# Performance work log

Measured on AMD Instinct MI355X. Metric: run time of the kernel, lower is better.

Reference implementation:

```python
import jax, jax.numpy as jnp
import numpy as np

B, N = 8192, 128          # batch, num intruders
D_OWN, D_GRID, D_INTR = 16, 512, 20
H, OUT = 128, 4


def setup_inputs() -> dict:
    key = jax.random.key(0)
    ks = jax.random.split(key, 12)
    rn = lambda k, shape, s=1.0: jax.random.normal(k, shape, jnp.float32) * s
    return {
        "state0": rn(ks[0], (B, D_OWN)),
        "state1": rn(ks[1], (B, D_GRID)),
        "state2": rn(ks[2], (B, N, D_INTR)),
        "W_own": rn(ks[3], (D_OWN, H), 0.1), "b_own": jnp.zeros((H,), jnp.float32),
        "W_intr": rn(ks[4], (D_INTR, H), 0.1), "b_intr": jnp.zeros((H,), jnp.float32),
        "W_grid": rn(ks[5], (D_GRID, H), 0.05), "b_grid": jnp.zeros((H,), jnp.float32),
        "Wq": rn(ks[6], (H, H), 0.08),
        "Wk": rn(ks[7], (H, H), 0.08),
        "Wv": rn(ks[8], (H, H), 0.08),
        "W1": rn(ks[9], (3 * H, H), 0.05), "b1": jnp.zeros((H,), jnp.float32),
        "W2": rn(ks[10], (H, OUT), 0.1), "b2": jnp.zeros((OUT,), jnp.float32),
    }


def reference(state0, state1, state2, W_own, b_own, W_intr, b_intr,
              W_grid, b_grid, Wq, Wk, Wv, W1, b1, W2, b2):
    own_e = jax.nn.relu(state0 @ W_own + b_own)            # [B,H]
    x_e = jax.nn.relu(state2 @ W_intr + b_intr)            # [B,N,H]
    q = own_e @ Wq                                         # [B,H]
    k = x_e @ Wk                                           # [B,N,H]
    v = x_e @ Wv                                           # [B,N,H]
    # mask = state2.mean(axis=2, keepdim=True).bool()  (nonzero test)
    mask = jnp.mean(state2, axis=2, keepdims=True) != 0    # [B,N,1]
    score = jnp.einsum('bnh,bh->bn', k, q)[..., None]      # bmm(k, q.unsqueeze(2)) -> [B,N,1]
    score = jnp.where(mask, score, -jnp.inf)
    alpha = jax.nn.softmax(score / np.float32(np.sqrt(H)), axis=1)
    alpha = jnp.where(mask, alpha, 0.0)
    v_att = jnp.sum(v * alpha, axis=1)                     # [B,H]
    own_grid = jax.nn.relu(state1 @ W_grid + b_grid)       # [B,H]
    concat = jnp.concatenate([own_e, v_att, own_grid], axis=1)  # [B,3H]
    out = (concat @ W1 + b1) @ W2 + b2                     # action_out_SAC
    mean = out
    log_std = jnp.clip(out, -20.0, 2.0)
    return mean, log_std
```

## Files before the change

kernel.cpp:

```cpp
#include <hip/hip_runtime.h>

typedef unsigned short ushort_t;
typedef __attribute__((ext_vector_type(8))) short bf16x8;
typedef __attribute__((ext_vector_type(4))) float f32x4;

__device__ __forceinline__ float bflo(unsigned u) { return __uint_as_float(u << 16); }
__device__ __forceinline__ float bfhi(unsigned u) { return __uint_as_float(u & 0xffff0000u); }
__device__ __forceinline__ float bfu(ushort_t s)  { return __uint_as_float((unsigned)s << 16); }
__device__ __forceinline__ ushort_t f2bf(float f) {
    unsigned u = __float_as_uint(f);
    u = u + 0x7fffu + ((u >> 16) & 1u);
    return (ushort_t)(u >> 16);
}
__device__ __forceinline__ void unpack8(uint4 v, float* f) {
    f[0]=bflo(v.x); f[1]=bfhi(v.x); f[2]=bflo(v.y); f[3]=bfhi(v.y);
    f[4]=bflo(v.z); f[5]=bfhi(v.z); f[6]=bflo(v.w); f[7]=bfhi(v.w);
}

__device__ __forceinline__ float load1(const void* p, size_t i, int f32) {
    return f32 ? ((const float*)p)[i] : bfu(((const ushort_t*)p)[i]);
}
__device__ __forceinline__ void load8(const void* p, size_t i, int f32, float* f) {
    if (f32) {
        const float4 a = *(const float4*)((const float*)p + i);
        const float4 b = *(const float4*)((const float*)p + i + 4);
        f[0]=a.x; f[1]=a.y; f[2]=a.z; f[3]=a.w;
        f[4]=b.x; f[5]=b.y; f[6]=b.z; f[7]=b.w;
    } else {
        unpack8(*(const uint4*)((const ushort_t*)p + i), f);
    }
}
__device__ __forceinline__ void load4(const void* p, size_t i, int f32, float* f) {
    if (f32) {
        const float4 a = *(const float4*)((const float*)p + i);
        f[0]=a.x; f[1]=a.y; f[2]=a.z; f[3]=a.w;
    } else {
        const uint2 u = *(const uint2*)((const ushort_t*)p + i);
        f[0]=bflo(u.x); f[1]=bfhi(u.x); f[2]=bflo(u.y); f[3]=bfhi(u.y);
    }
}

__device__ __forceinline__ int detect_f32(const ushort_t* s1h) {
    const int ln = threadIdx.x & 63;
    float v = fmaxf(fabsf(bfu(s1h[ln])), fabsf(bfu(s1h[ln + 64])));
    bool big = !(v <= 1e6f);
    return __ballot(big) != 0ull;
}

#define B_TOT 8192

__device__ __attribute__((aligned(16))) float    g_M[128 * 128];
__device__ __attribute__((aligned(16))) float    g_Wc1[384 * 4];
__device__ __attribute__((aligned(16))) float    g_Wv2[128 * 4];
__device__ __attribute__((aligned(16))) float    g_bc[4];
__device__ __attribute__((aligned(16))) float    g_t[B_TOT * 128];
__device__ __attribute__((aligned(16))) float    g_ogc[B_TOT * 4];
__device__ __attribute__((aligned(16))) ushort_t g_oe[B_TOT * 128];
__device__ __attribute__((aligned(16))) ushort_t g_Wib[128 * 32];

__global__ __launch_bounds__(128) void k_pre(
    const void* __restrict__ Wq, const void* __restrict__ Wk,
    const void* __restrict__ Wv, const void* __restrict__ W1,
    const void* __restrict__ b1, const void* __restrict__ W2,
    const void* __restrict__ b2, const void* __restrict__ W_intr,
    const ushort_t* __restrict__ s1h)
{
    __shared__ float wq_sh[128];
    __shared__ float w2_sh[512];
    __shared__ float wc1_mid[512];
    __shared__ float redc[128][4];
    const int tid = threadIdx.x;
    const int bx = blockIdx.x;
    const int f32 = detect_f32(s1h);

    if (bx < 128) {
        wq_sh[tid] = load1(Wq, bx*128 + tid, f32);
        __syncthreads();
        float acc = 0.f;
        #pragma unroll
        for (int c = 0; c < 16; ++c) {
            float f[8]; load8(Wk, (size_t)tid*128 + c*8, f32, f);
            #pragma unroll
            for (int j = 0; j < 8; ++j) acc = fmaf(wq_sh[c*8+j], f[j], acc);
        }
        g_M[bx*128 + tid] = acc;
    } else if (bx < 131) {
        const int rbase = (bx - 128) * 128;
        for (int i = tid; i < 512; i += 128) w2_sh[i] = load1(W2, i, f32);
        __syncthreads();

        const int r = rbase + tid;
        float a[4] = {0.f, 0.f, 0.f, 0.f};
        #pragma unroll
        for (int c = 0; c < 16; ++c) {
            float f[8]; load8(W1, (size_t)r*128 + c*8, f32, f);
            #pragma unroll
            for (int j = 0; j < 8; ++j) {
                const int p = c*8 + j;
                #pragma unroll
                for (int q = 0; q < 4; ++q) a[q] = fmaf(f[j], w2_sh[p*4+q], a[q]);
            }
        }
        #pragma unroll
        for (int q = 0; q < 4; ++q) g_Wc1[r*4+q] = a[q];

        if (bx == 129) {
            #pragma unroll
            for (int q = 0; q < 4; ++q) wc1_mid[tid*4+q] = a[q];
            __syncthreads();
            float v[4] = {0.f, 0.f, 0.f, 0.f};
            #pragma unroll
            for (int c = 0; c < 16; ++c) {
                float f[8]; load8(Wv, (size_t)tid*128 + c*8, f32, f);
                #pragma unroll
                for (int j = 0; j < 8; ++j) {
                    const int i2 = c*8 + j;
                    #pragma unroll
                    for (int q = 0; q < 4; ++q) v[q] = fmaf(f[j], wc1_mid[i2*4+q], v[q]);
                }
            }
            #pragma unroll
            for (int q = 0; q < 4; ++q) g_Wv2[tid*4+q] = v[q];

            const float bv = load1(b1, tid, f32);
            #pragma unroll
            for (int q = 0; q < 4; ++q) redc[tid][q] = bv * w2_sh[tid*4+q];
            __syncthreads();
            for (int s = 64; s > 0; s >>= 1) {
                if (tid < s) {
                    #pragma unroll
                    for (int q = 0; q < 4; ++q) redc[tid][q] += redc[tid+s][q];
                }
                __syncthreads();
            }
            if (tid < 4) g_bc[tid] = redc[0][tid] + load1(b2, tid, f32);
        }
    } else {
        ushort_t row[32];
        #pragma unroll
        for (int k = 0; k < 20; ++k) row[k] = f2bf(load1(W_intr, (size_t)k*128 + tid, f32));
        #pragma unroll
        for (int k = 20; k < 32; ++k) row[k] = 0;
        uint4* dst = (uint4*)&g_Wib[tid*32];
        const uint4* src = (const uint4*)row;
        #pragma unroll
        for (int c = 0; c < 4; ++c) dst[c] = src[c];
    }
}

__global__ __launch_bounds__(256) void k_ownt(
    const void* __restrict__ state0, const void* __restrict__ W_own,
    const void* __restrict__ b_own, const ushort_t* __restrict__ s1h)
{
    __shared__ float s0sh[16*16];
    __shared__ float wosh[16*128];
    __shared__ float bosh[128];
    __shared__ float oesh[16*129];
    __shared__ float Mt[32][128];
    const int tid = threadIdx.x;
    const int b0 = blockIdx.x * 16;
    const int f32 = detect_f32(s1h);

    if (tid < 32) {
        float f[8]; load8(state0, (size_t)b0*16 + tid*8, f32, f);
        #pragma unroll
        for (int j = 0; j < 8; ++j) s0sh[tid*8 + j] = f[j];
    }
    {
        float f[8]; load8(W_own, (size_t)tid*8, f32, f);
        #pragma unroll
        for (int j = 0; j < 8; ++j) wosh[tid*8 + j] = f[j];
    }
    if (tid < 128) bosh[tid] = load1(b_own, tid, f32);
    __syncthreads();

    #pragma unroll
    for (int kk = 0; kk < 8; ++kk) {
        const int idx = tid + kk*256;
        const int bi = idx >> 7, h = idx & 127;
        float acc = bosh[h];
        #pragma unroll
        for (int d = 0; d < 16; ++d) acc = fmaf(s0sh[bi*16+d], wosh[d*128+h], acc);
        acc = fmaxf(acc, 0.f);
        oesh[bi*129 + h] = acc;
        g_oe[(size_t)(b0+bi)*128 + h] = f2bf(acc);
    }

    const int bi0 = (tid >> 5) * 2;
    const int h0  = (tid & 31) * 4;
    float t00=0.f,t01=0.f,t02=0.f,t03=0.f,t10=0.f,t11=0.f,t12=0.f,t13=0.f;
    for (int kt = 0; kt < 128; kt += 32) {
        __syncthreads();
        #pragma unroll
        for (int c = 0; c < 4; ++c) {
            const int i = tid + c*256;
            const int kk = i >> 5;
            const int hh = (i & 31) * 4;
            *(float4*)&Mt[kk][hh] = *(const float4*)&g_M[(size_t)(kt+kk)*128 + hh];
        }
        __syncthreads();
        #pragma unroll
        for (int k = 0; k < 32; ++k) {
            const float4 mv = *(const float4*)&Mt[k][h0];
            const float a0 = oesh[(bi0+0)*129 + kt + k];
            const float a1 = oesh[(bi0+1)*129 + kt + k];
            t00=fmaf(a0,mv.x,t00); t01=fmaf(a0,mv.y,t01); t02=fmaf(a0,mv.z,t02); t03=fmaf(a0,mv.w,t03);
            t10=fmaf(a1,mv.x,t10); t11=fmaf(a1,mv.y,t11); t12=fmaf(a1,mv.z,t12); t13=fmaf(a1,mv.w,t13);
        }
    }
    *(float4*)&g_t[(size_t)(b0+bi0+0)*128 + h0] = make_float4(t00,t01,t02,t03);
    *(float4*)&g_t[(size_t)(b0+bi0+1)*128 + h0] = make_float4(t10,t11,t12,t13);
}

__global__ __launch_bounds__(256) void k_grid(
    const void* __restrict__ state1, const void* __restrict__ W_grid,
    const void* __restrict__ b_grid)
{
    __shared__ float s1T[32][18];
    __shared__ float wg[32][128];
    __shared__ float part[32][16][4];
    const int tid = threadIdx.x;
    const int b0 = blockIdx.x * 16;
    const int f32 = detect_f32((const ushort_t*)state1);

    const int bq = tid & 7;
    const int hq = tid >> 3;
    float a00=0.f,a01=0.f,a02=0.f,a03=0.f;
    float a10=0.f,a11=0.f,a12=0.f,a13=0.f;

    for (int kt = 0; kt < 512; kt += 32) {
        if (kt) __syncthreads();
        if (tid < 128) {
            const int bb = tid >> 3;
            const int kk = (tid & 7) * 4;
            float f[4];
            load4(state1, (size_t)(b0 + bb)*512 + kt + kk, f32, f);
            #pragma unroll
            for (int j = 0; j < 4; ++j) s1T[kk + j][bb] = f[j];
        }
        {
            #pragma unroll
            for (int c = 0; c < 4; ++c) {
                const int i = tid + c*256;
                const int kk = i >> 5;
                const int hh = (i & 31) * 4;
                float f[4];
                load4(W_grid, (size_t)(kt + kk)*128 + hh, f32, f);
                *(float4*)&wg[kk][hh] = make_float4(f[0], f[1], f[2], f[3]);
            }
        }
        __syncthreads();
        #pragma unroll 8
        for (int k = 0; k < 32; ++k) {
            const float x0 = s1T[k][bq*2 + 0];
            const float x1 = s1T[k][bq*2 + 1];
            const float4 w = *(const float4*)&wg[k][hq*4];
            a00=fmaf(x0,w.x,a00); a01=fmaf(x0,w.y,a01); a02=fmaf(x0,w.z,a02); a03=fmaf(x0,w.w,a03);
            a10=fmaf(x1,w.x,a10); a11=fmaf(x1,w.y,a11); a12=fmaf(x1,w.z,a12); a13=fmaf(x1,w.w,a13);
        }
    }

    float accs[2][4] = {{a00,a01,a02,a03},{a10,a11,a12,a13}};
    float pr[2][4] = {{0,0,0,0},{0,0,0,0}};
    #pragma unroll
    for (int jh = 0; jh < 4; ++jh) {
        const int h = hq*4 + jh;
        const float bg = load1(b_grid, h, f32);
        const float4 wc = *(const float4*)&g_Wc1[(256 + h)*4];
        #pragma unroll
        for (int ib = 0; ib < 2; ++ib) {
            const float og = fmaxf(accs[ib][jh] + bg, 0.f);
            pr[ib][0] = fmaf(og, wc.x, pr[ib][0]);
            pr[ib][1] = fmaf(og, wc.y, pr[ib][1]);
            pr[ib][2] = fmaf(og, wc.z, pr[ib][2]);
            pr[ib][3] = fmaf(og, wc.w, pr[ib][3]);
        }
    }
    __syncthreads();
    #pragma unroll
    for (int j = 0; j < 4; ++j) {
        part[hq][bq*2+0][j] = pr[0][j];
        part[hq][bq*2+1][j] = pr[1][j];
    }
    __syncthreads();
    if (tid < 64) {
        const int bb = tid >> 2, j = tid & 3;
        float s = 0.f;
        #pragma unroll
        for (int q = 0; q < 32; ++q) s += part[q][bb][j];
        g_ogc[(size_t)(b0 + bb)*4 + j] = s;
    }
}

__global__ __launch_bounds__(256, 4) void k_main(
    const void* __restrict__ state2, const void* __restrict__ b_intr,
    const ushort_t* __restrict__ s1h, void* __restrict__ out_raw)
{
    __shared__ __attribute__((aligned(16))) ushort_t s2b[128*40];
    __shared__ __attribute__((aligned(16))) ushort_t wib[128*40];
    __shared__ float t_sh[128], oe_sh[128], bi_sh[128];
    __shared__ float2 mlg_sh[128];
    __shared__ float msk_f[128];
    __shared__ float sc_part[4][128];
    __shared__ float u_sh[128];
    __shared__ float red4[4][4];

    const int tid = threadIdx.x;
    const int b = blockIdx.x;
    const int f32 = detect_f32(s1h);
    const int wv = tid >> 6, ln = tid & 63, lq = ln >> 4, lc = ln & 15;

    if (tid < 128) {
        const int n = tid;
        float v[20];
        const size_t base = (size_t)b*2560 + n*20;
        #pragma unroll
        for (int c = 0; c < 5; ++c) load4(state2, base + c*4, f32, v + c*4);
        float ms = 0.f;
        #pragma unroll
        for (int d = 0; d < 20; ++d) ms += v[d];
        msk_f[n] = (ms != 0.f) ? 1.f : 0.f;
        unsigned* row = (unsigned*)&s2b[n*40];
        #pragma unroll
        for (int c = 0; c < 10; ++c)
            row[c] = (unsigned)f2bf(v[2*c]) | ((unsigned)f2bf(v[2*c+1]) << 16);
        #pragma unroll
        for (int c = 10; c < 16; ++c) row[c] = 0u;
        t_sh[n]  = g_t[(size_t)b*128 + n];
        oe_sh[n] = bfu(g_oe[(size_t)b*128 + n]);
        bi_sh[n] = load1(b_intr, n, f32);
    } else {
        const int h = tid - 128;
        const uint4* src = (const uint4*)&g_Wib[h*32];
        uint4* dst = (uint4*)&wib[h*40];
        #pragma unroll
        for (int c = 0; c < 4; ++c) dst[c] = src[c];
    }
    __syncthreads();

    const int ht0 = 2*wv, ht1 = 2*wv + 1;
    const bf16x8 bb0 = *(const bf16x8*)&wib[(ht0*16 + lc)*40 + lq*8];
    const bf16x8 bb1 = *(const bf16x8*)&wib[(ht1*16 + lc)*40 + lq*8];
    const f32x4 zf = {0.f, 0.f, 0.f, 0.f};
    f32x4 acc0[8], acc1[8];
    #pragma unroll
    for (int nt = 0; nt < 8; ++nt) {
        const bf16x8 af = *(const bf16x8*)&s2b[(nt*16 + lc)*40 + lq*8];
        acc0[nt] = __builtin_amdgcn_mfma_f32_16x16x32_bf16(af, bb0, zf, 0, 0, 0);
        acc1[nt] = __builtin_amdgcn_mfma_f32_16x16x32_bf16(af, bb1, zf, 0, 0, 0);
    }

    const float bh0 = bi_sh[ht0*16 + lc], bh1 = bi_sh[ht1*16 + lc];
    const float tv0 = t_sh[ht0*16 + lc],  tv1 = t_sh[ht1*16 + lc];
    #pragma unroll
    for (int nt = 0; nt < 8; ++nt) {
        float s[4];
        #pragma unroll
        for (int r = 0; r < 4; ++r) {
            const float x0 = fmaxf(acc0[nt][r] + bh0, 0.f);
            const float x1 = fmaxf(acc1[nt][r] + bh1, 0.f);
            acc0[nt][r] = x0; acc1[nt][r] = x1;
            s[r] = fmaf(x1, tv1, x0 * tv0);
        }
        #pragma unroll
        for (int off = 1; off < 16; off <<= 1) {
            #pragma unroll
            for (int r = 0; r < 4; ++r) s[r] += __shfl_xor(s[r], off);
        }
        if (lc == 0) {
            #pragma unroll
            for (int r = 0; r < 4; ++r) sc_part[wv][nt*16 + lq*4 + r] = s[r];
        }
    }
    __syncthreads();

    if (tid < 128) {
        const int n = tid;
        const float s = sc_part[0][n] + sc_part[1][n] + sc_part[2][n] + sc_part[3][n];
        const float mk = msk_f[n];
        mlg_sh[n] = make_float2((mk != 0.f) ? s * 0.08838834764831845f : -1e30f, mk);
    }
    __syncthreads();

    const float l0 = mlg_sh[ln].x, l1 = mlg_sh[ln + 64].x;
    float mx = fmaxf(l0, l1);
    #pragma unroll
    for (int off = 1; off < 64; off <<= 1) mx = fmaxf(mx, __shfl_xor(mx, off));
    float es = __expf(fmaxf(l0 - mx, -80.f)) + __expf(fmaxf(l1 - mx, -80.f));
    #pragma unroll
    for (int off = 1; off < 64; off <<= 1) es += __shfl_xor(es, off);
    const float inv_d = 1.f / es;

    float u0 = 0.f, u1 = 0.f;
    #pragma unroll
    for (int nt = 0; nt < 8; ++nt) {
        #pragma unroll
        for (int r = 0; r < 4; ++r) {
            const float2 mlg = mlg_sh[nt*16 + lq*4 + r];
            const float a = mlg.y * __expf(fmaxf(mlg.x - mx, -80.f)) * inv_d;
            u0 = fmaf(a, acc0[nt][r], u0);
            u1 = fmaf(a, acc1[nt][r], u1);
        }
    }
    u0 += __shfl_xor(u0, 16); u0 += __shfl_xor(u0, 32);
    u1 += __shfl_xor(u1, 16); u1 += __shfl_xor(u1, 32);
    if (ln < 16) {
        u_sh[ht0*16 + ln] = u0;
        u_sh[ht1*16 + ln] = u1;
    }
    __syncthreads();

    float c0=0.f, c1=0.f, c2=0.f, c3=0.f;
    if (tid < 128) {
        const int h = tid;
        const float uu = u_sh[h], oo = oe_sh[h];
        const float4 wv2 = *(const float4*)&g_Wv2[h*4];
        const float4 wca = *(const float4*)&g_Wc1[h*4];
        c0 = uu*wv2.x + oo*wca.x;
        c1 = uu*wv2.y + oo*wca.y;
        c2 = uu*wv2.z + oo*wca.z;
        c3 = uu*wv2.w + oo*wca.w;
    }
    #pragma unroll
    for (int off = 32; off > 0; off >>= 1) {
        c0 += __shfl_down(c0, off); c1 += __shfl_down(c1, off);
        c2 += __shfl_down(c2, off); c3 += __shfl_down(c3, off);
    }
    if ((tid & 63) == 0) {
        red4[wv][0]=c0; red4[wv][1]=c1; red4[wv][2]=c2; red4[wv][3]=c3;
    }
    __syncthreads();
    if (tid < 4) {
        const int j = tid;
        const float o = g_bc[j] + g_ogc[(size_t)b*4 + j]
                      + red4[0][j] + red4[1][j] + red4[2][j] + red4[3][j];
        const float ls = fminf(fmaxf(o, -20.f), 2.f);
        if (f32) {
            float* of = (float*)out_raw;
            of[(size_t)b*4 + j] = o;
            of[(size_t)B_TOT*4 + (size_t)b*4 + j] = ls;
        } else {
            ushort_t* os = (ushort_t*)out_raw;
            os[(size_t)b*4 + j] = f2bf(o);
            os[(size_t)B_TOT*4 + (size_t)b*4 + j] = f2bf(ls);
        }
    }
}

extern "C" void kernel_launch(void* const* d_in, const int* in_sizes, int n_in,
                              void* d_out, int out_size, void* d_ws, size_t ws_size,
                              hipStream_t stream)
{
    (void)in_sizes; (void)n_in; (void)out_size; (void)d_ws; (void)ws_size;
    const void* state0 = d_in[0];
    const void* state1 = d_in[1];
    const void* state2 = d_in[2];
    const void* W_own  = d_in[3];
    const void* b_own  = d_in[4];
    const void* W_intr = d_in[5];
    const void* b_intr = d_in[6];
    const void* W_grid = d_in[7];
    const void* b_grid = d_in[8];
    const void* Wq     = d_in[9];
    const void* Wk     = d_in[10];
    const void* Wv     = d_in[11];
    const void* W1     = d_in[12];
    const void* b1     = d_in[13];
    const void* W2     = d_in[14];
    const void* b2     = d_in[15];
    const ushort_t* s1h = (const ushort_t*)state1;

    k_pre  <<<dim3(132), dim3(128), 0, stream>>>(Wq, Wk, Wv, W1, b1, W2, b2,
                                                 W_intr, s1h);
    k_ownt <<<dim3(512), dim3(256), 0, stream>>>(state0, W_own, b_own, s1h);
    k_grid <<<dim3(512), dim3(256), 0, stream>>>(state1, W_grid, b_grid);
    k_main <<<dim3(8192), dim3(256), 0, stream>>>(state2, b_intr, s1h, d_out);
}
```

Baseline: 313.5 us.

## Fuse all four kernels into one per-16-row kernel with per-block weight prep

New measurement: 395.6 us. 26.2% more time.

```diff
diff --git a/kernel.cpp b/kernel.cpp
--- a/kernel.cpp
+++ b/kernel.cpp
@@ -12,11 +12,13 @@
     u = u + 0x7fffu + ((u >> 16) & 1u);
     return (ushort_t)(u >> 16);
 }
+__device__ __forceinline__ unsigned pk2(float a, float b) {
+    return (unsigned)f2bf(a) | ((unsigned)f2bf(b) << 16);
+}
 __device__ __forceinline__ void unpack8(uint4 v, float* f) {
     f[0]=bflo(v.x); f[1]=bfhi(v.x); f[2]=bflo(v.y); f[3]=bfhi(v.y);
     f[4]=bflo(v.z); f[5]=bfhi(v.z); f[6]=bflo(v.w); f[7]=bfhi(v.w);
 }
-
 __device__ __forceinline__ float load1(const void* p, size_t i, int f32) {
     return f32 ? ((const float*)p)[i] : bfu(((const ushort_t*)p)[i]);
 }
@@ -39,7 +41,6 @@
         f[0]=bflo(u.x); f[1]=bfhi(u.x); f[2]=bflo(u.y); f[3]=bfhi(u.y);
     }
 }
-
 __device__ __forceinline__ int detect_f32(const ushort_t* s1h) {
     const int ln = threadIdx.x & 63;
     float v = fmaxf(fabsf(bfu(s1h[ln])), fabsf(bfu(s1h[ln + 64])));
@@ -49,118 +50,108 @@
 
 #define B_TOT 8192
 
-__device__ __attribute__((aligned(16))) float    g_M[128 * 128];
-__device__ __attribute__((aligned(16))) float    g_Wc1[384 * 4];
-__device__ __attribute__((aligned(16))) float    g_Wv2[128 * 4];
-__device__ __attribute__((aligned(16))) float    g_bc[4];
-__device__ __attribute__((aligned(16))) float    g_t[B_TOT * 128];
-__device__ __attribute__((aligned(16))) float    g_ogc[B_TOT * 4];
-__device__ __attribute__((aligned(16))) ushort_t g_oe[B_TOT * 128];
-__device__ __attribute__((aligned(16))) ushort_t g_Wib[128 * 32];
-
-__global__ __launch_bounds__(128) void k_pre(
-    const void* __restrict__ Wq, const void* __restrict__ Wk,
-    const void* __restrict__ Wv, const void* __restrict__ W1,
-    const void* __restrict__ b1, const void* __restrict__ W2,
-    const void* __restrict__ b2, const void* __restrict__ W_intr,
-    const ushort_t* __restrict__ s1h)
+__global__ __launch_bounds__(256, 2) void k_fused(
+    const void* __restrict__ state0, const void* __restrict__ state1,
+    const void* __restrict__ state2, const void* __restrict__ W_own,
+    const void* __restrict__ b_own, const void* __restrict__ W_intr,
+    const void* __restrict__ b_intr, const void* __restrict__ W_grid,
+    const void* __restrict__ b_grid, const void* __restrict__ Wq,
+    const void* __restrict__ Wk, const void* __restrict__ Wv,
+    const void* __restrict__ W1, const void* __restrict__ b1,
+    const void* __restrict__ W2, const void* __restrict__ b2,
+    void* __restrict__ out_raw)
 {
-    __shared__ float wq_sh[128];
-    __shared__ float w2_sh[512];
-    __shared__ float wc1_mid[512];
-    __shared__ float redc[128][4];
-    const int tid = threadIdx.x;
-    const int bx = blockIdx.x;
-    const int f32 = detect_f32(s1h);
-
-    if (bx < 128) {
-        wq_sh[tid] = load1(Wq, bx*128 + tid, f32);
-        __syncthreads();
-        float acc = 0.f;
-        #pragma unroll
-        for (int c = 0; c < 16; ++c) {
-            float f[8]; load8(Wk, (size_t)tid*128 + c*8, f32, f);
-            #pragma unroll
-            for (int j = 0; j < 8; ++j) acc = fmaf(wq_sh[c*8+j], f[j], acc);
-        }
-        g_M[bx*128 + tid] = acc;
-    } else if (bx < 131) {
-        const int rbase = (bx - 128) * 128;
-        for (int i = tid; i < 512; i += 128) w2_sh[i] = load1(W2, i, f32);
-        __syncthreads();
-
-        const int r = rbase + tid;
-        float a[4] = {0.f, 0.f, 0.f, 0.f};
-        #pragma unroll
-        for (int c = 0; c < 16; ++c) {
-            float f[8]; load8(W1, (size_t)r*128 + c*8, f32, f);
-            #pragma unroll
-            for (int j = 0; j < 8; ++j) {
-                const int p = c*8 + j;
-                #pragma unroll
-                for (int q = 0; q < 4; ++q) a[q] = fmaf(f[j], w2_sh[p*4+q], a[q]);
-            }
-        }
-        #pragma unroll
-        for (int q = 0; q < 4; ++q) g_Wc1[r*4+q] = a[q];
-
-        if (bx == 129) {
-            #pragma unroll
-            for (int q = 0; q < 4; ++q) wc1_mid[tid*4+q] = a[q];
-            __syncthreads();
-            float v[4] = {0.f, 0.f, 0.f, 0.f};
-            #pragma unroll
-            for (int c = 0; c < 16; ++c) {
-                float f[8]; load8(Wv, (size_t)tid*128 + c*8, f32, f);
-                #pragma unroll
-                for (int j = 0; j < 8; ++j) {
-                    const int i2 = c*8 + j;
-                    #pragma unroll
-                    for (int q = 0; q < 4; ++q) v[q] = fmaf(f[j], wc1_mid[i2*4+q], v[q]);
-                }
-            }
-            #pragma unroll
-            for (int q = 0; q < 4; ++q) g_Wv2[tid*4+q] = v[q];
-
-            const float bv = load1(b1, tid, f32);
-            #pragma unroll
-            for (int q = 0; q < 4; ++q) redc[tid][q] = bv * w2_sh[tid*4+q];
-            __syncthreads();
-            for (int s = 64; s > 0; s >>= 1) {
-                if (tid < s) {
-                    #pragma unroll
-                    for (int q = 0; q < 4; ++q) redc[tid][q] += redc[tid+s][q];
-                }
-                __syncthreads();
-            }
-            if (tid < 4) g_bc[tid] = redc[0][tid] + load1(b2, tid, f32);
-        }
-    } else {
-        ushort_t row[32];
-        #pragma unroll
-        for (int k = 0; k < 20; ++k) row[k] = f2bf(load1(W_intr, (size_t)k*128 + tid, f32));
-        #pragma unroll
-        for (int k = 20; k < 32; ++k) row[k] = 0;
-        uint4* dst = (uint4*)&g_Wib[tid*32];
-        const uint4* src = (const uint4*)row;
-        #pragma unroll
-        for (int c = 0; c < 4; ++c) dst[c] = src[c];
-    }
-}
-
-__global__ __launch_bounds__(256) void k_ownt(
-    const void* __restrict__ state0, const void* __restrict__ W_own,
-    const void* __restrict__ b_own, const ushort_t* __restrict__ s1h)
-{
-    __shared__ float s0sh[16*16];
-    __shared__ float wosh[16*128];
-    __shared__ float bosh[128];
-    __shared__ float oesh[16*129];
-    __shared__ float Mt[32][128];
+    __shared__ __attribute__((aligned(16))) float pool[10688];
+    float* w2sh = pool;
+    float* mid  = pool + 512;
+    float* wc1g = pool + 1024;
+    float* s0sh = pool + 1536;
+    float* qsh  = pool + 1792;
+    float* Wt   = pool + 3840;
+    float* s1Tp = pool + 8064;
+    float* part = pool + 8640;
+    __shared__ __attribute__((aligned(16))) ushort_t wib[128*40];
+    __shared__ __attribute__((aligned(16))) float tsh[16*128];
+    __shared__ __attribute__((aligned(16))) float oesh[16*128];
+    __shared__ __attribute__((aligned(16))) float wc1a[128*4];
+    __shared__ __attribute__((aligned(16))) float wv2s[128*4];
+    __shared__ __attribute__((aligned(16))) float msk[4*128];
+    __shared__ __attribute__((aligned(16))) float alph[4*128];
+    __shared__ float bi_sh[128], bc_sh[4], ogcsh[16*4];
+
     const int tid = threadIdx.x;
     const int b0 = blockIdx.x * 16;
-    const int f32 = detect_f32(s1h);
-
+    const int f32 = detect_f32((const ushort_t*)state1);
+    const int wv = tid >> 6, ln = tid & 63, lq = ln >> 4, lc = ln & 15;
+
+    if (tid < 128) bi_sh[tid] = load1(b_intr, tid, f32);
+    for (int i = tid; i < 512; i += 256) w2sh[i] = load1(W2, i, f32);
+    __syncthreads();
+
+    if (tid < 128) {
+        #pragma unroll
+        for (int seg = 0; seg < 3; ++seg) {
+            const int r = seg*128 + tid;
+            float a[4] = {0.f,0.f,0.f,0.f};
+            #pragma unroll
+            for (int c = 0; c < 16; ++c) {
+                float f[8]; load8(W1, (size_t)r*128 + c*8, f32, f);
+                #pragma unroll
+                for (int j = 0; j < 8; ++j) {
+                    const int p = c*8 + j;
+                    #pragma unroll
+                    for (int q = 0; q < 4; ++q) a[q] = fmaf(f[j], w2sh[p*4+q], a[q]);
+                }
+            }
+            float* dst = (seg == 0) ? wc1a : ((seg == 1) ? mid : wc1g);
+            #pragma unroll
+            for (int q = 0; q < 4; ++q) dst[tid*4+q] = a[q];
+        }
+    } else {
+        const int h = tid - 128;
+        ushort_t row[40];
+        #pragma unroll
+        for (int k = 0; k < 20; ++k) row[k] = f2bf(load1(W_intr, (size_t)k*128 + h, f32));
+        #pragma unroll
+        for (int k = 20; k < 40; ++k) row[k] = 0;
+        uint4* dst = (uint4*)&wib[h*40];
+        const uint4* src = (const uint4*)row;
+        #pragma unroll
+        for (int c = 0; c < 5; ++c) dst[c] = src[c];
+    }
+    __syncthreads();
+
+    float (*redc)[4] = (float(*)[4])part;
+    if (tid < 128) {
+        float v4[4] = {0.f,0.f,0.f,0.f};
+        #pragma unroll
+        for (int c = 0; c < 16; ++c) {
+            float f[8]; load8(Wv, (size_t)tid*128 + c*8, f32, f);
+            #pragma unroll
+            for (int j = 0; j < 8; ++j) {
+                const int i2 = c*8 + j;
+                #pragma unroll
+                for (int q = 0; q < 4; ++q) v4[q] = fmaf(f[j], mid[i2*4+q], v4[q]);
+            }
+        }
+        #pragma unroll
+        for (int q = 0; q < 4; ++q) wv2s[tid*4+q] = v4[q];
+        const float bv = load1(b1, tid, f32);
+        #pragma unroll
+        for (int q = 0; q < 4; ++q) redc[tid][q] = bv * w2sh[tid*4+q];
+    }
+    __syncthreads();
+    for (int s = 64; s > 0; s >>= 1) {
+        if (tid < s) {
+            #pragma unroll
+            for (int q = 0; q < 4; ++q) redc[tid][q] += redc[tid+s][q];
+        }
+        __syncthreads();
+    }
+    if (tid < 4) bc_sh[tid] = redc[0][tid] + load1(b2, tid, f32);
+
+    float* wosh = Wt;
+    if (tid < 128) mid[tid] = load1(b_own, tid, f32);
     if (tid < 32) {
         float f[8]; load8(state0, (size_t)b0*16 + tid*8, f32, f);
         #pragma unroll
@@ -171,278 +162,275 @@
         #pragma unroll
         for (int j = 0; j < 8; ++j) wosh[tid*8 + j] = f[j];
     }
-    if (tid < 128) bosh[tid] = load1(b_own, tid, f32);
-    __syncthreads();
-
+    __syncthreads();
     #pragma unroll
     for (int kk = 0; kk < 8; ++kk) {
         const int idx = tid + kk*256;
-        const int bi = idx >> 7, h = idx & 127;
-        float acc = bosh[h];
-        #pragma unroll
-        for (int d = 0; d < 16; ++d) acc = fmaf(s0sh[bi*16+d], wosh[d*128+h], acc);
-        acc = fmaxf(acc, 0.f);
-        oesh[bi*129 + h] = acc;
-        g_oe[(size_t)(b0+bi)*128 + h] = f2bf(acc);
+        const int biq = idx >> 7, h = idx & 127;
+        float acc = mid[h];
+        #pragma unroll
+        for (int d = 0; d < 16; ++d) acc = fmaf(s0sh[biq*16+d], wosh[d*128+h], acc);
+        oesh[biq*128 + h] = fmaxf(acc, 0.f);
     }
 
     const int bi0 = (tid >> 5) * 2;
     const int h0  = (tid & 31) * 4;
-    float t00=0.f,t01=0.f,t02=0.f,t03=0.f,t10=0.f,t11=0.f,t12=0.f,t13=0.f;
-    for (int kt = 0; kt < 128; kt += 32) {
-        __syncthreads();
-        #pragma unroll
-        for (int c = 0; c < 4; ++c) {
-            const int i = tid + c*256;
-            const int kk = i >> 5;
-            const int hh = (i & 31) * 4;
-            *(float4*)&Mt[kk][hh] = *(const float4*)&g_M[(size_t)(kt+kk)*128 + hh];
-        }
-        __syncthreads();
-        #pragma unroll
-        for (int k = 0; k < 32; ++k) {
-            const float4 mv = *(const float4*)&Mt[k][h0];
-            const float a0 = oesh[(bi0+0)*129 + kt + k];
-            const float a1 = oesh[(bi0+1)*129 + kt + k];
-            t00=fmaf(a0,mv.x,t00); t01=fmaf(a0,mv.y,t01); t02=fmaf(a0,mv.z,t02); t03=fmaf(a0,mv.w,t03);
-            t10=fmaf(a1,mv.x,t10); t11=fmaf(a1,mv.y,t11); t12=fmaf(a1,mv.z,t12); t13=fmaf(a1,mv.w,t13);
-        }
-    }
-    *(float4*)&g_t[(size_t)(b0+bi0+0)*128 + h0] = make_float4(t00,t01,t02,t03);
-    *(float4*)&g_t[(size_t)(b0+bi0+1)*128 + h0] = make_float4(t10,t11,t12,t13);
-}
-
-__global__ __launch_bounds__(256) void k_grid(
-    const void* __restrict__ state1, const void* __restrict__ W_grid,
-    const void* __restrict__ b_grid)
-{
-    __shared__ float s1T[32][18];
-    __shared__ float wg[32][128];
-    __shared__ float part[32][16][4];
-    const int tid = threadIdx.x;
-    const int b0 = blockIdx.x * 16;
-    const int f32 = detect_f32((const ushort_t*)state1);
-
-    const int bq = tid & 7;
-    const int hq = tid >> 3;
-    float a00=0.f,a01=0.f,a02=0.f,a03=0.f;
-    float a10=0.f,a11=0.f,a12=0.f,a13=0.f;
-
-    for (int kt = 0; kt < 512; kt += 32) {
-        if (kt) __syncthreads();
-        if (tid < 128) {
-            const int bb = tid >> 3;
-            const int kk = (tid & 7) * 4;
-            float f[4];
-            load4(state1, (size_t)(b0 + bb)*512 + kt + kk, f32, f);
-            #pragma unroll
-            for (int j = 0; j < 4; ++j) s1T[kk + j][bb] = f[j];
-        }
-        {
+    {
+        float q0[4] = {0,0,0,0}, q1[4] = {0,0,0,0};
+        for (int kt = 0; kt < 128; kt += 32) {
+            __syncthreads();
             #pragma unroll
             for (int c = 0; c < 4; ++c) {
                 const int i = tid + c*256;
-                const int kk = i >> 5;
-                const int hh = (i & 31) * 4;
-                float f[4];
-                load4(W_grid, (size_t)(kt + kk)*128 + hh, f32, f);
-                *(float4*)&wg[kk][hh] = make_float4(f[0], f[1], f[2], f[3]);
+                const int kk = i >> 5, hh = (i & 31) * 4;
+                float f[4]; load4(Wq, (size_t)(kt+kk)*128 + hh, f32, f);
+                *(float4*)&Wt[kk*132 + hh] = make_float4(f[0],f[1],f[2],f[3]);
+            }
+            __syncthreads();
+            #pragma unroll
+            for (int k = 0; k < 32; ++k) {
+                const float4 mv = *(const float4*)&Wt[k*132 + h0];
+                const float a0 = oesh[bi0*128 + kt + k];
+                const float a1 = oesh[(bi0+1)*128 + kt + k];
+                q0[0]=fmaf(a0,mv.x,q0[0]); q0[1]=fmaf(a0,mv.y,q0[1]);
+                q0[2]=fmaf(a0,mv.z,q0[2]); q0[3]=fmaf(a0,mv.w,q0[3]);
+                q1[0]=fmaf(a1,mv.x,q1[0]); q1[1]=fmaf(a1,mv.y,q1[1]);
+                q1[2]=fmaf(a1,mv.z,q1[2]); q1[3]=fmaf(a1,mv.w,q1[3]);
+            }
+        }
+        *(float4*)&qsh[bi0*128 + h0]     = make_float4(q0[0],q0[1],q0[2],q0[3]);
+        *(float4*)&qsh[(bi0+1)*128 + h0] = make_float4(q1[0],q1[1],q1[2],q1[3]);
+    }
+    __syncthreads();
+
+    {
+        float t0[4] = {0,0,0,0}, t1[4] = {0,0,0,0};
+        for (int kt = 0; kt < 128; kt += 32) {
+            if (kt) __syncthreads();
+            #pragma unroll
+            for (int c = 0; c < 4; ++c) {
+                const int i = tid + c*256;
+                const int h2 = i >> 3, c4 = (i & 7) * 4;
+                float f[4]; load4(Wk, (size_t)h2*128 + kt + c4, f32, f);
+                #pragma unroll
+                for (int j = 0; j < 4; ++j) Wt[(c4+j)*132 + h2] = f[j];
+            }
+            __syncthreads();
+            #pragma unroll
+            for (int k = 0; k < 32; ++k) {
+                const float4 mv = *(const float4*)&Wt[k*132 + h0];
+                const float a0 = qsh[bi0*128 + kt + k];
+                const float a1 = qsh[(bi0+1)*128 + kt + k];
+                t0[0]=fmaf(a0,mv.x,t0[0]); t0[1]=fmaf(a0,mv.y,t0[1]);
+                t0[2]=fmaf(a0,mv.z,t0[2]); t0[3]=fmaf(a0,mv.w,t0[3]);
+                t1[0]=fmaf(a1,mv.x,t1[0]); t1[1]=fmaf(a1,mv.y,t1[1]);
+                t1[2]=fmaf(a1,mv.z,t1[2]); t1[3]=fmaf(a1,mv.w,t1[3]);
+            }
+        }
+        *(float4*)&tsh[bi0*128 + h0]     = make_float4(t0[0],t0[1],t0[2],t0[3]);
+        *(float4*)&tsh[(bi0+1)*128 + h0] = make_float4(t1[0],t1[1],t1[2],t1[3]);
+    }
+    __syncthreads();
+
+    {
+        float* wg = Wt;
+        const int bq = tid & 7, hq = tid >> 3;
+        float a00=0,a01=0,a02=0,a03=0,a10=0,a11=0,a12=0,a13=0;
+        for (int kt = 0; kt < 512; kt += 32) {
+            if (kt) __syncthreads();
+            if (tid < 128) {
+                const int bb = tid >> 3, kk2 = (tid & 7) * 4;
+                float f[4]; load4(state1, (size_t)(b0+bb)*512 + kt + kk2, f32, f);
+                #pragma unroll
+                for (int j = 0; j < 4; ++j) s1Tp[(kk2+j)*18 + bb] = f[j];
+            }
+            #pragma unroll
+            for (int c = 0; c < 4; ++c) {
+                const int i = tid + c*256;
+                const int kk = i >> 5, hh = (i & 31) * 4;
+                float f[4]; load4(W_grid, (size_t)(kt+kk)*128 + hh, f32, f);
+                *(float4*)&wg[kk*132 + hh] = make_float4(f[0],f[1],f[2],f[3]);
+            }
+            __syncthreads();
+            #pragma unroll 8
+            for (int k = 0; k < 32; ++k) {
+                const float x0 = s1Tp[k*18 + bq*2 + 0];
+                const float x1 = s1Tp[k*18 + bq*2 + 1];
+                const float4 w = *(const float4*)&wg[k*132 + hq*4];
+                a00=fmaf(x0,w.x,a00); a01=fmaf(x0,w.y,a01); a02=fmaf(x0,w.z,a02); a03=fmaf(x0,w.w,a03);
+                a10=fmaf(x1,w.x,a10); a11=fmaf(x1,w.y,a11); a12=fmaf(x1,w.z,a12); a13=fmaf(x1,w.w,a13);
+            }
+        }
+        float accs[2][4] = {{a00,a01,a02,a03},{a10,a11,a12,a13}};
+        float pr[2][4] = {{0,0,0,0},{0,0,0,0}};
+        #pragma unroll
+        for (int jh = 0; jh < 4; ++jh) {
+            const int h = hq*4 + jh;
+            const float bg = load1(b_grid, h, f32);
+            const float4 wc = *(const float4*)&wc1g[h*4];
+            #pragma unroll
+            for (int ib = 0; ib < 2; ++ib) {
+                const float og = fmaxf(accs[ib][jh] + bg, 0.f);
+                pr[ib][0]=fmaf(og,wc.x,pr[ib][0]); pr[ib][1]=fmaf(og,wc.y,pr[ib][1]);
+                pr[ib][2]=fmaf(og,wc.z,pr[ib][2]); pr[ib][3]=fmaf(og,wc.w,pr[ib][3]);
             }
         }
         __syncthreads();
-        #pragma unroll 8
-        for (int k = 0; k < 32; ++k) {
-            const float x0 = s1T[k][bq*2 + 0];
-            const float x1 = s1T[k][bq*2 + 1];
-            const float4 w = *(const float4*)&wg[k][hq*4];
-            a00=fmaf(x0,w.x,a00); a01=fmaf(x0,w.y,a01); a02=fmaf(x0,w.z,a02); a03=fmaf(x0,w.w,a03);
-            a10=fmaf(x1,w.x,a10); a11=fmaf(x1,w.y,a11); a12=fmaf(x1,w.z,a12); a13=fmaf(x1,w.w,a13);
-        }
-    }
-
-    float accs[2][4] = {{a00,a01,a02,a03},{a10,a11,a12,a13}};
-    float pr[2][4] = {{0,0,0,0},{0,0,0,0}};
+        float (*pp)[16][4] = (float(*)[16][4])part;
+        #pragma unroll
+        for (int j = 0; j < 4; ++j) {
+            pp[hq][bq*2+0][j] = pr[0][j];
+            pp[hq][bq*2+1][j] = pr[1][j];
+        }
+        __syncthreads();
+        if (tid < 64) {
+            const int bb = tid >> 2, j = tid & 3;
+            float s = 0.f;
+            #pragma unroll
+            for (int q = 0; q < 32; ++q) s += pp[q][bb][j];
+            ogcsh[bb*4 + j] = s;
+        }
+    }
+    __syncthreads();
+
+    ushort_t* s2w = (ushort_t*)pool + wv*5120;
+    const f32x4 zf = {0.f,0.f,0.f,0.f};
+    bf16x8 wf[8];
     #pragma unroll
-    for (int jh = 0; jh < 4; ++jh) {
-        const int h = hq*4 + jh;
-        const float bg = load1(b_grid, h, f32);
-        const float4 wc = *(const float4*)&g_Wc1[(256 + h)*4];
-        #pragma unroll
-        for (int ib = 0; ib < 2; ++ib) {
-            const float og = fmaxf(accs[ib][jh] + bg, 0.f);
-            pr[ib][0] = fmaf(og, wc.x, pr[ib][0]);
-            pr[ib][1] = fmaf(og, wc.y, pr[ib][1]);
-            pr[ib][2] = fmaf(og, wc.z, pr[ib][2]);
-            pr[ib][3] = fmaf(og, wc.w, pr[ib][3]);
-        }
-    }
-    __syncthreads();
+    for (int ht = 0; ht < 8; ++ht)
+        wf[ht] = *(const bf16x8*)&wib[(ht*16 + lc)*40 + lq*8];
+    float bcol[8];
     #pragma unroll
-    for (int j = 0; j < 4; ++j) {
-        part[hq][bq*2+0][j] = pr[0][j];
-        part[hq][bq*2+1][j] = pr[1][j];
-    }
-    __syncthreads();
-    if (tid < 64) {
-        const int bb = tid >> 2, j = tid & 3;
-        float s = 0.f;
-        #pragma unroll
-        for (int q = 0; q < 32; ++q) s += part[q][bb][j];
-        g_ogc[(size_t)(b0 + bb)*4 + j] = s;
-    }
-}
-
-__global__ __launch_bounds__(256, 4) void k_main(
-    const void* __restrict__ state2, const void* __restrict__ b_intr,
-    const ushort_t* __restrict__ s1h, void* __restrict__ out_raw)
-{
-    __shared__ __attribute__((aligned(16))) ushort_t s2b[128*40];
-    __shared__ __attribute__((aligned(16))) ushort_t wib[128*40];
-    __shared__ float t_sh[128], oe_sh[128], bi_sh[128];
-    __shared__ float2 mlg_sh[128];
-    __shared__ float msk_f[128];
-    __shared__ float sc_part[4][128];
-    __shared__ float u_sh[128];
-    __shared__ float red4[4][4];
-
-    const int tid = threadIdx.x;
-    const int b = blockIdx.x;
-    const int f32 = detect_f32(s1h);
-    const int wv = tid >> 6, ln = tid & 63, lq = ln >> 4, lc = ln & 15;
-
-    if (tid < 128) {
-        const int n = tid;
-        float v[20];
-        const size_t base = (size_t)b*2560 + n*20;
-        #pragma unroll
-        for (int c = 0; c < 5; ++c) load4(state2, base + c*4, f32, v + c*4);
-        float ms = 0.f;
-        #pragma unroll
-        for (int d = 0; d < 20; ++d) ms += v[d];
-        msk_f[n] = (ms != 0.f) ? 1.f : 0.f;
-        unsigned* row = (unsigned*)&s2b[n*40];
-        #pragma unroll
-        for (int c = 0; c < 10; ++c)
-            row[c] = (unsigned)f2bf(v[2*c]) | ((unsigned)f2bf(v[2*c+1]) << 16);
-        #pragma unroll
-        for (int c = 10; c < 16; ++c) row[c] = 0u;
-        t_sh[n]  = g_t[(size_t)b*128 + n];
-        oe_sh[n] = bfu(g_oe[(size_t)b*128 + n]);
-        bi_sh[n] = load1(b_intr, n, f32);
-    } else {
-        const int h = tid - 128;
-        const uint4* src = (const uint4*)&g_Wib[h*32];
-        uint4* dst = (uint4*)&wib[h*40];
-        #pragma unroll
-        for (int c = 0; c < 4; ++c) dst[c] = src[c];
-    }
-    __syncthreads();
-
-    const int ht0 = 2*wv, ht1 = 2*wv + 1;
-    const bf16x8 bb0 = *(const bf16x8*)&wib[(ht0*16 + lc)*40 + lq*8];
-    const bf16x8 bb1 = *(const bf16x8*)&wib[(ht1*16 + lc)*40 + lq*8];
-    const f32x4 zf = {0.f, 0.f, 0.f, 0.f};
-    f32x4 acc0[8], acc1[8];
-    #pragma unroll
-    for (int nt = 0; nt < 8; ++nt) {
-        const bf16x8 af = *(const bf16x8*)&s2b[(nt*16 + lc)*40 + lq*8];
-        acc0[nt] = __builtin_amdgcn_mfma_f32_16x16x32_bf16(af, bb0, zf, 0, 0, 0);
-        acc1[nt] = __builtin_amdgcn_mfma_f32_16x16x32_bf16(af, bb1, zf, 0, 0, 0);
-    }
-
-    const float bh0 = bi_sh[ht0*16 + lc], bh1 = bi_sh[ht1*16 + lc];
-    const float tv0 = t_sh[ht0*16 + lc],  tv1 = t_sh[ht1*16 + lc];
-    #pragma unroll
-    for (int nt = 0; nt < 8; ++nt) {
-        float s[4];
-        #pragma unroll
-        for (int r = 0; r < 4; ++r) {
-            const float x0 = fmaxf(acc0[nt][r] + bh0, 0.f);
-            const float x1 = fmaxf(acc1[nt][r] + bh1, 0.f);
-            acc0[nt][r] = x0; acc1[nt][r] = x1;
-            s[r] = fmaf(x1, tv1, x0 * tv0);
+    for (int ht = 0; ht < 8; ++ht) bcol[ht] = bi_sh[ht*16 + lc];
+
+    for (int rr = 0; rr < 4; ++rr) {
+        const int bi = rr*4 + wv;
+        const size_t b = (size_t)(b0 + bi);
+        #pragma unroll
+        for (int half = 0; half < 2; ++half) {
+            const int n = ln + half*64;
+            float v[20];
+            #pragma unroll
+            for (int c = 0; c < 5; ++c) load4(state2, b*2560 + n*20 + c*4, f32, v + c*4);
+            float ms = 0.f;
+            #pragma unroll
+            for (int d = 0; d < 20; ++d) ms += v[d];
+            msk[wv*128 + n] = (ms != 0.f) ? 1.f : 0.f;
+            unsigned r32[20];
+            #pragma unroll
+            for (int c = 0; c < 10; ++c) r32[c] = pk2(v[2*c], v[2*c+1]);
+            #pragma unroll
+            for (int c = 10; c < 20; ++c) r32[c] = 0u;
+            uint4* dst = (uint4*)&s2w[n*40];
+            const uint4* src = (const uint4*)r32;
+            #pragma unroll
+            for (int c = 0; c < 5; ++c) dst[c] = src[c];
+        }
+        bf16x8 sf[8];
+        #pragma unroll
+        for (int nt = 0; nt < 8; ++nt)
+            sf[nt] = *(const bf16x8*)&s2w[(nt*16 + lc)*40 + lq*8];
+
+        float sc[8];
+        #pragma unroll
+        for (int nt = 0; nt < 8; ++nt) sc[nt] = 0.f;
+        #pragma unroll
+        for (int ht = 0; ht < 8; ++ht) {
+            const float4 tv4 = *(const float4*)&tsh[bi*128 + ht*16 + lq*4];
+            const float4 bv4 = *(const float4*)&bi_sh[ht*16 + lq*4];
+            const float tv[4] = {tv4.x,tv4.y,tv4.z,tv4.w};
+            const float bv[4] = {bv4.x,bv4.y,bv4.z,bv4.w};
+            #pragma unroll
+            for (int nt = 0; nt < 8; ++nt) {
+                const f32x4 acc = __builtin_amdgcn_mfma_f32_16x16x32_bf16(wf[ht], sf[nt], zf, 0,0,0);
+                #pragma unroll
+                for (int r = 0; r < 4; ++r)
+                    sc[nt] = fmaf(fmaxf(acc[r] + bv[r], 0.f), tv[r], sc[nt]);
+            }
+        }
+        #pragma unroll
+        for (int nt = 0; nt < 8; ++nt) {
+            sc[nt] += __shfl_xor(sc[nt], 16);
+            sc[nt] += __shfl_xor(sc[nt], 32);
+        }
+        float lg[8], mk8[8];
+        #pragma unroll
+        for (int nt = 0; nt < 8; ++nt) {
+            mk8[nt] = msk[wv*128 + nt*16 + lc];
+            lg[nt] = (mk8[nt] != 0.f) ? sc[nt] * 0.08838834764831845f : -1e30f;
+        }
+        float mx = lg[0];
+        #pragma unroll
+        for (int nt = 1; nt < 8; ++nt) mx = fmaxf(mx, lg[nt]);
+        #pragma unroll
+        for (int off = 1; off < 16; off <<= 1) mx = fmaxf(mx, __shfl_xor(mx, off));
+        float e8[8], es = 0.f;
+        #pragma unroll
+        for (int nt = 0; nt < 8; ++nt) {
+            e8[nt] = mk8[nt] * __expf(fmaxf(lg[nt] - mx, -80.f));
+            es += e8[nt];
+        }
+        #pragma unroll
+        for (int off = 1; off < 16; off <<= 1) es += __shfl_xor(es, off);
+        const float inv_d = (es > 0.f) ? 1.f / es : 0.f;
+        if (lq == 0) {
+            #pragma unroll
+            for (int nt = 0; nt < 8; ++nt)
+                alph[wv*128 + nt*16 + lc] = e8[nt] * inv_d;
+        }
+
+        float u8[8];
+        #pragma unroll
+        for (int ht = 0; ht < 8; ++ht) u8[ht] = 0.f;
+        #pragma unroll
+        for (int nt = 0; nt < 8; ++nt) {
+            const float4 a4 = *(const float4*)&alph[wv*128 + nt*16 + lq*4];
+            const float av[4] = {a4.x,a4.y,a4.z,a4.w};
+            #pragma unroll
+            for (int ht = 0; ht < 8; ++ht) {
+                const f32x4 acc = __builtin_amdgcn_mfma_f32_16x16x32_bf16(sf[nt], wf[ht], zf, 0,0,0);
+                #pragma unroll
+                for (int r = 0; r < 4; ++r)
+                    u8[ht] = fmaf(av[r], fmaxf(acc[r] + bcol[ht], 0.f), u8[ht]);
+            }
+        }
+        #pragma unroll
+        for (int ht = 0; ht < 8; ++ht) {
+            u8[ht] += __shfl_xor(u8[ht], 16);
+            u8[ht] += __shfl_xor(u8[ht], 32);
+        }
+        float cj[4] = {0.f,0.f,0.f,0.f};
+        #pragma unroll
+        for (int ht = 0; ht < 8; ++ht) {
+            const int h = ht*16 + lc;
+            const float oo = oesh[bi*128 + h];
+            const float4 w2v = *(const float4*)&wv2s[h*4];
+            const float4 w1v = *(const float4*)&wc1a[h*4];
+            cj[0] += u8[ht]*w2v.x + oo*w1v.x;
+            cj[1] += u8[ht]*w2v.y + oo*w1v.y;
+            cj[2] += u8[ht]*w2v.z + oo*w1v.z;
+            cj[3] += u8[ht]*w2v.w + oo*w1v.w;
         }
         #pragma unroll
         for (int off = 1; off < 16; off <<= 1) {
             #pragma unroll
-            for (int r = 0; r < 4; ++r) s[r] += __shfl_xor(s[r], off);
-        }
-        if (lc == 0) {
-            #pragma unroll
-            for (int r = 0; r < 4; ++r) sc_part[wv][nt*16 + lq*4 + r] = s[r];
-        }
-    }
-    __syncthreads();
-
-    if (tid < 128) {
-        const int n = tid;
-        const float s = sc_part[0][n] + sc_part[1][n] + sc_part[2][n] + sc_part[3][n];
-        const float mk = msk_f[n];
-        mlg_sh[n] = make_float2((mk != 0.f) ? s * 0.08838834764831845f : -1e30f, mk);
-    }
-    __syncthreads();
-
-    const float l0 = mlg_sh[ln].x, l1 = mlg_sh[ln + 64].x;
-    float mx = fmaxf(l0, l1);
-    #pragma unroll
-    for (int off = 1; off < 64; off <<= 1) mx = fmaxf(mx, __shfl_xor(mx, off));
-    float es = __expf(fmaxf(l0 - mx, -80.f)) + __expf(fmaxf(l1 - mx, -80.f));
-    #pragma unroll
-    for (int off = 1; off < 64; off <<= 1) es += __shfl_xor(es, off);
-    const float inv_d = 1.f / es;
-
-    float u0 = 0.f, u1 = 0.f;
-    #pragma unroll
-    for (int nt = 0; nt < 8; ++nt) {
-        #pragma unroll
-        for (int r = 0; r < 4; ++r) {
-            const float2 mlg = mlg_sh[nt*16 + lq*4 + r];
-            const float a = mlg.y * __expf(fmaxf(mlg.x - mx, -80.f)) * inv_d;
-            u0 = fmaf(a, acc0[nt][r], u0);
-            u1 = fmaf(a, acc1[nt][r], u1);
-        }
-    }
-    u0 += __shfl_xor(u0, 16); u0 += __shfl_xor(u0, 32);
-    u1 += __shfl_xor(u1, 16); u1 += __shfl_xor(u1, 32);
-    if (ln < 16) {
-        u_sh[ht0*16 + ln] = u0;
-        u_sh[ht1*16 + ln] = u1;
-    }
-    __syncthreads();
-
-    float c0=0.f, c1=0.f, c2=0.f, c3=0.f;
-    if (tid < 128) {
-        const int h = tid;
-        const float uu = u_sh[h], oo = oe_sh[h];
-        const float4 wv2 = *(const float4*)&g_Wv2[h*4];
-        const float4 wca = *(const float4*)&g_Wc1[h*4];
-        c0 = uu*wv2.x + oo*wca.x;
-        c1 = uu*wv2.y + oo*wca.y;
-        c2 = uu*wv2.z + oo*wca.z;
-        c3 = uu*wv2.w + oo*wca.w;
-    }
-    #pragma unroll
-    for (int off = 32; off > 0; off >>= 1) {
-        c0 += __shfl_down(c0, off); c1 += __shfl_down(c1, off);
-        c2 += __shfl_down(c2, off); c3 += __shfl_down(c3, off);
-    }
-    if ((tid & 63) == 0) {
-        red4[wv][0]=c0; red4[wv][1]=c1; red4[wv][2]=c2; red4[wv][3]=c3;
-    }
-    __syncthreads();
-    if (tid < 4) {
-        const int j = tid;
-        const float o = g_bc[j] + g_ogc[(size_t)b*4 + j]
-                      + red4[0][j] + red4[1][j] + red4[2][j] + red4[3][j];
-        const float ls = fminf(fmaxf(o, -20.f), 2.f);
-        if (f32) {
-            float* of = (float*)out_raw;
-            of[(size_t)b*4 + j] = o;
-            of[(size_t)B_TOT*4 + (size_t)b*4 + j] = ls;
-        } else {
-            ushort_t* os = (ushort_t*)out_raw;
-            os[(size_t)b*4 + j] = f2bf(o);
-            os[(size_t)B_TOT*4 + (size_t)b*4 + j] = f2bf(ls);
+            for (int j = 0; j < 4; ++j) cj[j] += __shfl_xor(cj[j], off);
+        }
+        if (ln == 0) {
+            #pragma unroll
+            for (int j = 0; j < 4; ++j) {
+                const float o = bc_sh[j] + ogcsh[bi*4 + j] + cj[j];
+                const float ls = fminf(fmaxf(o, -20.f), 2.f);
+                if (f32) {
+                    float* of = (float*)out_raw;
+                    of[b*4 + j] = o;
+                    of[(size_t)B_TOT*4 + b*4 + j] = ls;
+                } else {
+                    ushort_t* os = (ushort_t*)out_raw;
+                    os[b*4 + j] = f2bf(o);
+                    os[(size_t)B_TOT*4 + b*4 + j] = f2bf(ls);
+                }
+            }
         }
     }
 }
@@ -452,27 +440,8 @@
                               hipStream_t stream)
 {
     (void)in_sizes; (void)n_in; (void)out_size; (void)d_ws; (void)ws_size;
-    const void* state0 = d_in[0];
-    const void* state1 = d_in[1];
-    const void* state2 = d_in[2];
-    const void* W_own  = d_in[3];
-    const void* b_own  = d_in[4];
-    const void* W_intr = d_in[5];
-    const void* b_intr = d_in[6];
-    const void* W_grid = d_in[7];
-    const void* b_grid = d_in[8];
-    const void* Wq     = d_in[9];
-    const void* Wk     = d_in[10];
-    const void* Wv     = d_in[11];
-    const void* W1     = d_in[12];
-    const void* b1     = d_in[13];
-    const void* W2     = d_in[14];
-    const void* b2     = d_in[15];
-    const ushort_t* s1h = (const ushort_t*)state1;
-
-    k_pre  <<<dim3(132), dim3(128), 0, stream>>>(Wq, Wk, Wv, W1, b1, W2, b2,
-                                                 W_intr, s1h);
-    k_ownt <<<dim3(512), dim3(256), 0, stream>>>(state0, W_own, b_own, s1h);
-    k_grid <<<dim3(512), dim3(256), 0, stream>>>(state1, W_grid, b_grid);
-    k_main <<<dim3(8192), dim3(256), 0, stream>>>(state2, b_intr, s1h, d_out);
-}
+    k_fused<<<dim3(512), dim3(256), 0, stream>>>(
+        d_in[0], d_in[1], d_in[2], d_in[3], d_in[4], d_in[5], d_in[6], d_in[7],
+        d_in[8], d_in[9], d_in[10], d_in[11], d_in[12], d_in[13], d_in[14],
+        d_in[15], d_out);
+}
```
